# Kernel tuning notes

Hardware: AMD Instinct MI355X
Metric: run time of the kernel (lower is better)

## Reference

```python
import jax, jax.numpy as jnp
import numpy as np


def setup_inputs() -> dict:
    key = jax.random.key(0)
    k1, k2 = jax.random.split(key)
    z_e_x = jax.random.normal(k1, (4096, 16, 128), dtype=jnp.float32)
    codebook = jax.random.normal(k2, (1024, 128), dtype=jnp.float32)
    return {"z_e_x": z_e_x, "codebook": codebook}


def reference(z_e_x, codebook):
    # VQStraightThrough.forward: nearest-codebook quantization in fp32.
    B, N, C = z_e_x.shape
    x = z_e_x.astype(jnp.float32).reshape(B * N, C)          # [BN, C]
    cb = codebook.astype(jnp.float32)                        # [K, C]
    inputs_sq = jnp.sum(x * x, axis=1, keepdims=True)        # [BN, 1]
    codebook_sq = jnp.sum(cb * cb, axis=1)                   # [K]
    l2_dis = inputs_sq + codebook_sq - 2.0 * (x @ cb.T)      # [BN, K]
    flat_idx = jnp.argmin(l2_dis, axis=1)                    # [BN] int
    min_vals = jnp.min(l2_dis, axis=1)                       # [BN]
    idx = flat_idx.reshape(B, N)
    distances = min_vals.reshape(B, N).astype(z_e_x.dtype)
    codes = cb[flat_idx].reshape(B, N, C).astype(z_e_x.dtype)  # gather
    return codes, flat_idx, idx, distances
```

## Files before the change

kernel.cpp:

```cpp
#include <hip/hip_runtime.h>
#include <math.h>
#include <stdint.h>

#define C        128
#define KCODES   1024
#define TPB      256
#define ROWS_PB  128
#define NCHUNK   64
#define NCHUNKS  (KCODES / NCHUNK)
#define BSTRIDE  272
#define BHALF    (NCHUNK * BSTRIDE)
#define EPS_TRIG 0.25f

typedef __attribute__((ext_vector_type(8))) short bf16x8_t;
typedef __attribute__((ext_vector_type(4))) float f32x4_t;

static __device__ __forceinline__ uint32_t bf16_rne(float f) {
    uint32_t u = __float_as_uint(f);
    return (u + 0x7FFFu + ((u >> 16) & 1u)) >> 16;
}
static __device__ __forceinline__ float bf16_hi_f(float f) {
    return __uint_as_float(bf16_rne(f) << 16);
}

#define SLOTS(OP) OP(0,0) OP(0,1) OP(0,2) OP(0,3) OP(1,0) OP(1,1) OP(1,2) OP(1,3)
#define MFMA_BF16 __builtin_amdgcn_mfma_f32_16x16x32_bf16

__global__ __launch_bounds__(TPB, 3)
void vq_fused_kernel(const float* __restrict__ x,
                     const float* __restrict__ cb,
                     float* __restrict__ out_codes,
                     float* __restrict__ out_fidx,
                     float* __restrict__ out_idx,
                     float* __restrict__ out_dist,
                     int rows)
{
    __shared__ __align__(16) uint8_t s_buf[2 * BHALF];
    __shared__ float s_cq[NCHUNK];
    __shared__ float s_v1[ROWS_PB], s_v2[ROWS_PB];
    __shared__ int   s_k1[ROWS_PB], s_k2[ROWS_PB];

    const int t    = threadIdx.x;
    const int lane = t & 63;
    const int w    = t >> 6;
    const int ln   = lane & 15;
    const int quad = lane >> 4;
    const int rowblock = blockIdx.x * ROWS_PB;

    #pragma unroll 4
    for (int i = 0; i < 16; ++i) {
        int fid = t + i * TPB;
        int row = fid >> 5;
        int kq  = fid & 31;
        int grow = rowblock + row;
        grow = grow < rows ? grow : rows - 1;
        float4 v = ((const float4*)x)[(size_t)grow * 32 + kq];
        uint32_t p0 = bf16_rne(v.x) | (bf16_rne(v.y) << 16);
        uint32_t p1 = bf16_rne(v.z) | (bf16_rne(v.w) << 16);
        *(uint2*)(s_buf + row * BSTRIDE + kq * 8) = make_uint2(p0, p1);
    }
    __syncthreads();

    const int arow0 = (w * 32 + ln) * BSTRIDE;
    const int arow1 = (w * 32 + 16 + ln) * BSTRIDE;
    bf16x8_t ah00, ah01, ah02, ah03, ah10, ah11, ah12, ah13;
    ah00 = *(const bf16x8_t*)(s_buf + arow0 + 0 * 64 + quad * 16);
    ah01 = *(const bf16x8_t*)(s_buf + arow0 + 1 * 64 + quad * 16);
    ah02 = *(const bf16x8_t*)(s_buf + arow0 + 2 * 64 + quad * 16);
    ah03 = *(const bf16x8_t*)(s_buf + arow0 + 3 * 64 + quad * 16);
    ah10 = *(const bf16x8_t*)(s_buf + arow1 + 0 * 64 + quad * 16);
    ah11 = *(const bf16x8_t*)(s_buf + arow1 + 1 * 64 + quad * 16);
    ah12 = *(const bf16x8_t*)(s_buf + arow1 + 2 * 64 + quad * 16);
    ah13 = *(const bf16x8_t*)(s_buf + arow1 + 3 * 64 + quad * 16);
    __syncthreads();

    #pragma unroll 4
    for (int i = 0; i < 16; ++i) {
        int fid = t + i * TPB;
        int row = fid >> 5;
        int kq  = fid & 31;
        int grow = rowblock + row;
        grow = grow < rows ? grow : rows - 1;
        float4 v = ((const float4*)x)[(size_t)grow * 32 + kq];
        uint32_t p0 = bf16_rne(v.x - bf16_hi_f(v.x)) | (bf16_rne(v.y - bf16_hi_f(v.y)) << 16);
        uint32_t p1 = bf16_rne(v.z - bf16_hi_f(v.z)) | (bf16_rne(v.w - bf16_hi_f(v.w)) << 16);
        *(uint2*)(s_buf + row * BSTRIDE + kq * 8) = make_uint2(p0, p1);
    }
    __syncthreads();

    bf16x8_t al00, al01, al02, al03, al10, al11, al12, al13;
    al00 = *(const bf16x8_t*)(s_buf + arow0 + 0 * 64 + quad * 16);
    al01 = *(const bf16x8_t*)(s_buf + arow0 + 1 * 64 + quad * 16);
    al02 = *(const bf16x8_t*)(s_buf + arow0 + 2 * 64 + quad * 16);
    al03 = *(const bf16x8_t*)(s_buf + arow0 + 3 * 64 + quad * 16);
    al10 = *(const bf16x8_t*)(s_buf + arow1 + 0 * 64 + quad * 16);
    al11 = *(const bf16x8_t*)(s_buf + arow1 + 1 * 64 + quad * 16);
    al12 = *(const bf16x8_t*)(s_buf + arow1 + 2 * 64 + quad * 16);
    al13 = *(const bf16x8_t*)(s_buf + arow1 + 3 * 64 + quad * 16);
    __syncthreads();

#define DECL(g,r) float v1_##g##r = INFINITY, v2_##g##r = INFINITY; int k1_##g##r = 0, k2_##g##r = 0;
    SLOTS(DECL)
#undef DECL

    #pragma unroll 1
    for (int chn = 0; chn < NCHUNKS; ++chn) {
        const int kbase = chn * NCHUNK;
        #pragma unroll
        for (int i = 0; i < 4; ++i) {
            int uid  = t + i * TPB;
            int code = uid >> 4, g = uid & 15;
            const float4* src = (const float4*)(cb + (size_t)(kbase + code) * C) + g * 2;
            float4 v0 = src[0], v1 = src[1];
            uint32_t h0 = bf16_rne(v0.x) | (bf16_rne(v0.y) << 16);
            uint32_t h1 = bf16_rne(v0.z) | (bf16_rne(v0.w) << 16);
            uint32_t h2 = bf16_rne(v1.x) | (bf16_rne(v1.y) << 16);
            uint32_t h3 = bf16_rne(v1.z) | (bf16_rne(v1.w) << 16);
            uint32_t l0 = bf16_rne(v0.x - bf16_hi_f(v0.x)) | (bf16_rne(v0.y - bf16_hi_f(v0.y)) << 16);
            uint32_t l1 = bf16_rne(v0.z - bf16_hi_f(v0.z)) | (bf16_rne(v0.w - bf16_hi_f(v0.w)) << 16);
            uint32_t l2 = bf16_rne(v1.x - bf16_hi_f(v1.x)) | (bf16_rne(v1.y - bf16_hi_f(v1.y)) << 16);
            uint32_t l3 = bf16_rne(v1.z - bf16_hi_f(v1.z)) | (bf16_rne(v1.w - bf16_hi_f(v1.w)) << 16);
            *(uint4*)(s_buf + code * BSTRIDE + g * 16)          = make_uint4(h0, h1, h2, h3);
            *(uint4*)(s_buf + BHALF + code * BSTRIDE + g * 16)  = make_uint4(l0, l1, l2, l3);
            float ps = ((v0.x * v0.x + v0.y * v0.y) + (v0.z * v0.z + v0.w * v0.w))
                     + ((v1.x * v1.x + v1.y * v1.y) + (v1.z * v1.z + v1.w * v1.w));
            ps += __shfl_xor(ps, 1, 16);
            ps += __shfl_xor(ps, 2, 16);
            ps += __shfl_xor(ps, 4, 16);
            ps += __shfl_xor(ps, 8, 16);
            if (g == 0) s_cq[code] = ps;
        }
        __syncthreads();

        const uint8_t* bbase = s_buf + (size_t)ln * BSTRIDE + quad * 16;
        #pragma unroll
        for (int ct = 0; ct < 4; ++ct) {
            const uint8_t* bh_p = bbase + (size_t)ct * 16 * BSTRIDE;
            const uint8_t* bl_p = bh_p + BHALF;
            f32x4_t acc0 = {0.f, 0.f, 0.f, 0.f};
            f32x4_t acc1 = {0.f, 0.f, 0.f, 0.f};
#define KSTEP(kk) { \
            bf16x8_t bh = *(const bf16x8_t*)(bh_p + kk * 64); \
            bf16x8_t bl = *(const bf16x8_t*)(bl_p + kk * 64); \
            acc0 = MFMA_BF16(ah0##kk, bh, acc0, 0, 0, 0); \
            acc0 = MFMA_BF16(al0##kk, bh, acc0, 0, 0, 0); \
            acc0 = MFMA_BF16(ah0##kk, bl, acc0, 0, 0, 0); \
            acc1 = MFMA_BF16(ah1##kk, bh, acc1, 0, 0, 0); \
            acc1 = MFMA_BF16(al1##kk, bh, acc1, 0, 0, 0); \
            acc1 = MFMA_BF16(ah1##kk, bl, acc1, 0, 0, 0); }
            KSTEP(0) KSTEP(1) KSTEP(2) KSTEP(3)
#undef KSTEP
            const float cqv = s_cq[ct * 16 + ln];
            const int   kc  = kbase + ct * 16 + ln;
#define UPD(g,r) { \
            float s_ = fmaf(-2.0f, (g ? acc1 : acc0)[r], cqv); \
            bool c1_ = s_ < v1_##g##r; \
            bool c2_ = s_ < v2_##g##r; \
            v2_##g##r = c1_ ? v1_##g##r : (c2_ ? s_ : v2_##g##r); \
            k2_##g##r = c1_ ? k1_##g##r : (c2_ ? kc : k2_##g##r); \
            v1_##g##r = c1_ ? s_ : v1_##g##r; \
            k1_##g##r = c1_ ? kc : k1_##g##r; }
            SLOTS(UPD)
#undef UPD
        }
        __syncthreads();
    }

    for (int m_ = 1; m_ <= 8; m_ <<= 1) {
#define MRG(g,r) { \
        float ov1 = __shfl_xor(v1_##g##r, m_, 16); int ok1 = __shfl_xor(k1_##g##r, m_, 16); \
        float ov2 = __shfl_xor(v2_##g##r, m_, 16); int ok2 = __shfl_xor(k2_##g##r, m_, 16); \
        if (ov1 < v1_##g##r || (ov1 == v1_##g##r && ok1 < k1_##g##r)) { \
            if (v1_##g##r < ov2 || (v1_##g##r == ov2 && k1_##g##r < ok2)) { v2_##g##r = v1_##g##r; k2_##g##r = k1_##g##r; } \
            else { v2_##g##r = ov2; k2_##g##r = ok2; } \
            v1_##g##r = ov1; k1_##g##r = ok1; \
        } else if (ov1 < v2_##g##r || (ov1 == v2_##g##r && ok1 < k2_##g##r)) { \
            v2_##g##r = ov1; k2_##g##r = ok1; \
        } }
        SLOTS(MRG)
#undef MRG
    }
    if (ln == 0) {
#define WRT(g,r) { int rloc = w * 32 + g * 16 + quad * 4 + r; \
        s_v1[rloc] = v1_##g##r; s_v2[rloc] = v2_##g##r; \
        s_k1[rloc] = k1_##g##r; s_k2[rloc] = k2_##g##r; }
        SLOTS(WRT)
#undef WRT
    }
    __syncthreads();

    if (t < ROWS_PB) {
        int rowg = rowblock + t;
        const bool valid = rowg < rows;
        rowg = valid ? rowg : rows - 1;
        float v1 = s_v1[t], v2 = s_v2[t];
        int k1 = s_k1[t], k2 = s_k2[t];
        const float* xr = x + (size_t)rowg * C;

        float sx = 0.f, sy = 0.f, sz = 0.f, sw = 0.f;
        {
            const float4* xp = (const float4*)xr;
            #pragma unroll
            for (int i = 0; i < C / 4; ++i) {
                float4 v = xp[i];
                sx += v.x * v.x; sy += v.y * v.y;
                sz += v.z * v.z; sw += v.w * v.w;
            }
        }
        const float rs = (sx + sy) + (sz + sw);

        bool switched = false;
        double qwin = 0.0;
        if (v2 - v1 < EPS_TRIG) {
            const float* c1p = cb + (size_t)k1 * C;
            const float* c2p = cb + (size_t)k2 * C;
            double dot1 = 0.0, cq1 = 0.0, dot2 = 0.0, cq2 = 0.0;
            #pragma unroll 8
            for (int c = 0; c < C; ++c) {
                const double xc  = (double)xr[c];
                const double cv1 = (double)c1p[c];
                const double cv2 = (double)c2p[c];
                dot1 += xc * cv1;  cq1 += cv1 * cv1;
                dot2 += xc * cv2;  cq2 += cv2 * cv2;
            }
            const double q1 = cq1 - 2.0 * dot1;
            const double q2 = cq2 - 2.0 * dot2;
            if (q2 < q1 || (q2 == q1 && k2 < k1)) { k1 = k2; switched = true; qwin = q2; }
        }

        {
            const float4* c1p4 = (const float4*)(cb + (size_t)k1 * C);
            float a = 0.f;
            float qx = 0.f, qy = 0.f, qz = 0.f, qw = 0.f;
            #pragma unroll
            for (int i = 0; i < C / 4; ++i) {
                float4 cv = c1p4[i];
                float4 xv = ((const float4*)xr)[i];
                a = fmaf(xv.x, cv.x, a); a = fmaf(xv.y, cv.y, a);
                a = fmaf(xv.z, cv.z, a); a = fmaf(xv.w, cv.w, a);
                qx += cv.x * cv.x; qy += cv.y * cv.y;
                qz += cv.z * cv.z; qw += cv.w * cv.w;
            }
            float d = (rs + ((qx + qy) + (qz + qw))) - 2.f * a;
            if (switched) d = (float)((double)rs + qwin);

            if (valid) {
                out_fidx[rowg] = (float)k1;
                out_idx[rowg]  = (float)k1;
                out_dist[rowg] = d;
            }
        }
        s_k1[t] = k1;
    }
    __syncthreads();

    {
        const int r    = t >> 1;
        const int half = t & 1;
        const int rowg = rowblock + r;
        if (rowg < rows) {
            const int k1 = s_k1[r];
            const float4* src = (const float4*)(cb + (size_t)k1 * C) + half * 16;
            float4*       dst = (float4*)(out_codes + (size_t)rowg * C) + half * 16;
            #pragma unroll
            for (int i = 0; i < 16; ++i) dst[i] = src[i];
        }
    }
}

extern "C" void kernel_launch(void* const* d_in, const int* in_sizes, int n_in,
                              void* d_out, int out_size, void* d_ws, size_t ws_size,
                              hipStream_t stream) {
    const float* x  = (const float*)d_in[0];
    const float* cb = (const float*)d_in[1];
    const int rows = in_sizes[0] / C;

    float* out       = (float*)d_out;
    float* out_codes = out;
    float* out_fidx  = out + (size_t)rows * C;
    float* out_idx   = out_fidx + rows;
    float* out_dist  = out_idx + rows;

    const int grid = (rows + ROWS_PB - 1) / ROWS_PB;
    vq_fused_kernel<<<grid, TPB, 0, stream>>>(x, cb, out_codes, out_fidx,
                                              out_idx, out_dist, rows);
}
```

Measured before the change: 184.7 us.

## Split codebook search across two wave groups per block and merge top-2

Doubles the block to 512 threads and splits the codebook into two halves, so each group of four waves scans 512 codes against the same 128 rows using its own shared-memory buffer. The per-half top-2 candidates are merged in shared memory before the refinement and gather steps, which now use four threads per row. The aim is more waves per block to hide MFMA and load latency and halve the serial chunk loop per wave. In exchange it doubles LDS use per block (about 70KB), which may limit how many blocks fit per CU, and the raised launch-bound occupancy target may add register pressure.

```diff
diff --git a/kernel.cpp b/kernel.cpp
--- a/kernel.cpp
+++ b/kernel.cpp
@@ -4,12 +4,14 @@
 
 #define C        128
 #define KCODES   1024
-#define TPB      256
+#define KHALF    512
+#define TPB      512
 #define ROWS_PB  128
 #define NCHUNK   64
-#define NCHUNKS  (KCODES / NCHUNK)
+#define NCHUNKS_H (KHALF / NCHUNK)
 #define BSTRIDE  272
 #define BHALF    (NCHUNK * BSTRIDE)
+#define BUFB     (2 * BHALF)
 #define EPS_TRIG 0.25f
 
 typedef __attribute__((ext_vector_type(8))) short bf16x8_t;
@@ -26,7 +28,7 @@
 #define SLOTS(OP) OP(0,0) OP(0,1) OP(0,2) OP(0,3) OP(1,0) OP(1,1) OP(1,2) OP(1,3)
 #define MFMA_BF16 __builtin_amdgcn_mfma_f32_16x16x32_bf16
 
-__global__ __launch_bounds__(TPB, 3)
+__global__ __launch_bounds__(TPB, 4)
 void vq_fused_kernel(const float* __restrict__ x,
                      const float* __restrict__ cb,
                      float* __restrict__ out_codes,
@@ -35,20 +37,25 @@
                      float* __restrict__ out_dist,
                      int rows)
 {
-    __shared__ __align__(16) uint8_t s_buf[2 * BHALF];
-    __shared__ float s_cq[NCHUNK];
-    __shared__ float s_v1[ROWS_PB], s_v2[ROWS_PB];
-    __shared__ int   s_k1[ROWS_PB], s_k2[ROWS_PB];
+    __shared__ __align__(16) uint8_t s_buf[2 * BUFB];
+    __shared__ float s_cq[2][NCHUNK];
+    __shared__ float s_v1h[2][ROWS_PB], s_v2h[2][ROWS_PB];
+    __shared__ int   s_k1h[2][ROWS_PB], s_k2h[2][ROWS_PB];
+    __shared__ int   s_k1f[ROWS_PB];
 
     const int t    = threadIdx.x;
     const int lane = t & 63;
     const int w    = t >> 6;
+    const int kh   = w >> 2;
+    const int wg   = w & 3;
+    const int tg   = t & 255;
     const int ln   = lane & 15;
     const int quad = lane >> 4;
     const int rowblock = blockIdx.x * ROWS_PB;
+    const int kh0      = kh * KHALF;
 
     #pragma unroll 4
-    for (int i = 0; i < 16; ++i) {
+    for (int i = 0; i < 8; ++i) {
         int fid = t + i * TPB;
         int row = fid >> 5;
         int kq  = fid & 31;
@@ -61,8 +68,8 @@
     }
     __syncthreads();
 
-    const int arow0 = (w * 32 + ln) * BSTRIDE;
-    const int arow1 = (w * 32 + 16 + ln) * BSTRIDE;
+    const int arow0 = (wg * 32 + ln) * BSTRIDE;
+    const int arow1 = (wg * 32 + 16 + ln) * BSTRIDE;
     bf16x8_t ah00, ah01, ah02, ah03, ah10, ah11, ah12, ah13;
     ah00 = *(const bf16x8_t*)(s_buf + arow0 + 0 * 64 + quad * 16);
     ah01 = *(const bf16x8_t*)(s_buf + arow0 + 1 * 64 + quad * 16);
@@ -75,7 +82,7 @@
     __syncthreads();
 
     #pragma unroll 4
-    for (int i = 0; i < 16; ++i) {
+    for (int i = 0; i < 8; ++i) {
         int fid = t + i * TPB;
         int row = fid >> 5;
         int kq  = fid & 31;
@@ -103,12 +110,14 @@
     SLOTS(DECL)
 #undef DECL
 
+    uint8_t* const gbuf = s_buf + kh * BUFB;
+
     #pragma unroll 1
-    for (int chn = 0; chn < NCHUNKS; ++chn) {
-        const int kbase = chn * NCHUNK;
+    for (int chn = 0; chn < NCHUNKS_H; ++chn) {
+        const int kbase = kh0 + chn * NCHUNK;
         #pragma unroll
         for (int i = 0; i < 4; ++i) {
-            int uid  = t + i * TPB;
+            int uid  = tg + i * 256;
             int code = uid >> 4, g = uid & 15;
             const float4* src = (const float4*)(cb + (size_t)(kbase + code) * C) + g * 2;
             float4 v0 = src[0], v1 = src[1];
@@ -120,19 +129,19 @@
             uint32_t l1 = bf16_rne(v0.z - bf16_hi_f(v0.z)) | (bf16_rne(v0.w - bf16_hi_f(v0.w)) << 16);
             uint32_t l2 = bf16_rne(v1.x - bf16_hi_f(v1.x)) | (bf16_rne(v1.y - bf16_hi_f(v1.y)) << 16);
             uint32_t l3 = bf16_rne(v1.z - bf16_hi_f(v1.z)) | (bf16_rne(v1.w - bf16_hi_f(v1.w)) << 16);
-            *(uint4*)(s_buf + code * BSTRIDE + g * 16)          = make_uint4(h0, h1, h2, h3);
-            *(uint4*)(s_buf + BHALF + code * BSTRIDE + g * 16)  = make_uint4(l0, l1, l2, l3);
+            *(uint4*)(gbuf + code * BSTRIDE + g * 16)          = make_uint4(h0, h1, h2, h3);
+            *(uint4*)(gbuf + BHALF + code * BSTRIDE + g * 16)  = make_uint4(l0, l1, l2, l3);
             float ps = ((v0.x * v0.x + v0.y * v0.y) + (v0.z * v0.z + v0.w * v0.w))
                      + ((v1.x * v1.x + v1.y * v1.y) + (v1.z * v1.z + v1.w * v1.w));
             ps += __shfl_xor(ps, 1, 16);
             ps += __shfl_xor(ps, 2, 16);
             ps += __shfl_xor(ps, 4, 16);
             ps += __shfl_xor(ps, 8, 16);
-            if (g == 0) s_cq[code] = ps;
+            if (g == 0) s_cq[kh][code] = ps;
         }
         __syncthreads();
 
-        const uint8_t* bbase = s_buf + (size_t)ln * BSTRIDE + quad * 16;
+        const uint8_t* bbase = gbuf + (size_t)ln * BSTRIDE + quad * 16;
         #pragma unroll
         for (int ct = 0; ct < 4; ++ct) {
             const uint8_t* bh_p = bbase + (size_t)ct * 16 * BSTRIDE;
@@ -150,7 +159,7 @@
             acc1 = MFMA_BF16(ah1##kk, bl, acc1, 0, 0, 0); }
             KSTEP(0) KSTEP(1) KSTEP(2) KSTEP(3)
 #undef KSTEP
-            const float cqv = s_cq[ct * 16 + ln];
+            const float cqv = s_cq[kh][ct * 16 + ln];
             const int   kc  = kbase + ct * 16 + ln;
 #define UPD(g,r) { \
             float s_ = fmaf(-2.0f, (g ? acc1 : acc0)[r], cqv); \
@@ -181,9 +190,9 @@
 #undef MRG
     }
     if (ln == 0) {
-#define WRT(g,r) { int rloc = w * 32 + g * 16 + quad * 4 + r; \
-        s_v1[rloc] = v1_##g##r; s_v2[rloc] = v2_##g##r; \
-        s_k1[rloc] = k1_##g##r; s_k2[rloc] = k2_##g##r; }
+#define WRT(g,r) { int rloc = wg * 32 + g * 16 + quad * 4 + r; \
+        s_v1h[kh][rloc] = v1_##g##r; s_v2h[kh][rloc] = v2_##g##r; \
+        s_k1h[kh][rloc] = k1_##g##r; s_k2h[kh][rloc] = k2_##g##r; }
         SLOTS(WRT)
 #undef WRT
     }
@@ -193,8 +202,23 @@
         int rowg = rowblock + t;
         const bool valid = rowg < rows;
         rowg = valid ? rowg : rows - 1;
-        float v1 = s_v1[t], v2 = s_v2[t];
-        int k1 = s_k1[t], k2 = s_k2[t];
+
+        float av1 = s_v1h[0][t], av2 = s_v2h[0][t];
+        int   ak1 = s_k1h[0][t], ak2 = s_k2h[0][t];
+        float bv1 = s_v1h[1][t], bv2 = s_v2h[1][t];
+        int   bk1 = s_k1h[1][t], bk2 = s_k2h[1][t];
+
+        float v1, v2; int k1, k2;
+        if (bv1 < av1 || (bv1 == av1 && bk1 < ak1)) {
+            v1 = bv1; k1 = bk1;
+            if (av1 < bv2 || (av1 == bv2 && ak1 < bk2)) { v2 = av1; k2 = ak1; }
+            else                                        { v2 = bv2; k2 = bk2; }
+        } else {
+            v1 = av1; k1 = ak1;
+            if (bv1 < av2 || (bv1 == av2 && bk1 < ak2)) { v2 = bv1; k2 = bk1; }
+            else                                        { v2 = av2; k2 = ak2; }
+        }
+
         const float* xr = x + (size_t)rowg * C;
 
         float sx = 0.f, sy = 0.f, sz = 0.f, sw = 0.f;
@@ -250,20 +274,20 @@
                 out_dist[rowg] = d;
             }
         }
-        s_k1[t] = k1;
+        s_k1f[t] = k1;
     }
     __syncthreads();
 
     {
-        const int r    = t >> 1;
-        const int half = t & 1;
+        const int r   = t >> 2;
+        const int sub = t & 3;
         const int rowg = rowblock + r;
         if (rowg < rows) {
-            const int k1 = s_k1[r];
-            const float4* src = (const float4*)(cb + (size_t)k1 * C) + half * 16;
-            float4*       dst = (float4*)(out_codes + (size_t)rowg * C) + half * 16;
+            const int k1 = s_k1f[r];
+            const float4* src = (const float4*)(cb + (size_t)k1 * C) + sub * 8;
+            float4*       dst = (float4*)(out_codes + (size_t)rowg * C) + sub * 8;
             #pragma unroll
-            for (int i = 0; i < 16; ++i) dst[i] = src[i];
+            for (int i = 0; i < 8; ++i) dst[i] = src[i];
         }
     }
 }
```

Result: slower. 312.7 us (+69.3%).
